# Performance work log

Measured on AMD Instinct MI355X. Metric: run time of the kernel, lower is better.

Reference implementation:

```python
import jax, jax.numpy as jnp
import numpy as np

ALPHA = 0.2  # leaky relu slope
NEG_BIG = -9000000000000000.0


def setup_inputs() -> dict:
    key = jax.random.key(0)
    k1, k2, k3, k4 = jax.random.split(key, 4)
    B, N, Fin, Fout = 8, 2048, 256, 256
    h = jax.random.normal(k1, (B, N, Fin), dtype=jnp.float32)
    adj = jax.random.randint(k2, (B, N, N), 0, 2, dtype=jnp.int32)
    # xavier_uniform with gain=1.414
    gain = 1.414
    limW = gain * np.sqrt(6.0 / (Fin + Fout))
    W = jax.random.uniform(k3, (Fin, Fout), dtype=jnp.float32, minval=-limW, maxval=limW)
    lima = gain * np.sqrt(6.0 / (2 * Fout + 1))
    a = jax.random.uniform(k4, (2 * Fout, 1), dtype=jnp.float32, minval=-lima, maxval=lima)
    return {"h": h, "adj": adj, "W": W, "a": a}


def reference(h, adj, W, a):
    # Wh: [B, N, F]
    Wh = jnp.matmul(h, W)
    Fout = W.shape[1]
    a1 = a[:Fout, 0]   # scores for source node i (repeat_interleave side)
    a2 = a[Fout:, 0]   # scores for target node j (repeat side)
    # e[b,i,j] = leakyrelu(Wh[b,i]@a1 + Wh[b,j]@a2)  -- decomposed, no O(N^2 * 2F) tensor
    s1 = jnp.einsum('bnf,f->bn', Wh, a1)  # [B, N]
    s2 = jnp.einsum('bnf,f->bn', Wh, a2)  # [B, N]
    e = jax.nn.leaky_relu(s1[:, :, None] + s2[:, None, :], negative_slope=ALPHA)
    masked = jnp.where(adj > 0, e, jnp.full_like(e, NEG_BIG))
    attention = jax.nn.softmax(masked, axis=2)  # dropout=0 (eval mode)
    h_prime = jnp.matmul(attention, Wh)  # [B, N, F]
    return jax.nn.elu(h_prime)
```

## Files before the change

kernel.cpp:

```cpp
#include <hip/hip_runtime.h>

typedef __attribute__((ext_vector_type(8))) short bhalf8;
typedef __attribute__((ext_vector_type(4))) float floatx4;

#define ALPHA_LR 0.2f

__device__ __forceinline__ unsigned short f2bf(float f) {
  union { float f; unsigned int u; } v; v.f = f;
  unsigned int r = v.u + 0x7fffu + ((v.u >> 16) & 1u);
  return (unsigned short)(r >> 16);
}
__device__ __forceinline__ float bf2f(unsigned short u) {
  union { unsigned int u; float f; } v; v.u = ((unsigned int)u) << 16;
  return v.f;
}
__device__ __forceinline__ void gld16(const void* g, void* l) {
  __builtin_amdgcn_global_load_lds((const __attribute__((address_space(1))) unsigned int*)g,
                                   (__attribute__((address_space(3))) unsigned int*)l,
                                   16, 0, 0);
}

__global__ void k0w_split(const float* __restrict__ W,
                          unsigned short* __restrict__ WThi,
                          unsigned short* __restrict__ WTlo,
                          unsigned int* __restrict__ s2maxEnc) {
  __shared__ float s[16][17];
  const int tx = threadIdx.x, ty = threadIdx.y;
  if (blockIdx.x == 0 && blockIdx.y == 0 && ty == 0 && tx < 8) s2maxEnc[tx] = 0u;
  const int n0 = blockIdx.x * 16, k0 = blockIdx.y * 16;
  s[ty][tx] = W[(k0 + ty) * 256 + n0 + tx];
  __syncthreads();
  float v = s[tx][ty];
  const int k = k0 + tx, n = n0 + ty;
  unsigned short hi = f2bf(v);
  unsigned short lo = f2bf(v - bf2f(hi));
  const int idx = (k >> 5) * 8192 + n * 32 + (k & 31);
  WThi[idx] = hi;
  WTlo[idx] = lo;
}

__global__ __launch_bounds__(512, 2) void k1_mfma(const float* __restrict__ h,
                                                  const unsigned short* __restrict__ Bhi_g,
                                                  const unsigned short* __restrict__ Blo_g,
                                                  const float* __restrict__ a_g,
                                                  unsigned short* __restrict__ WhPack,
                                                  float* __restrict__ s1,
                                                  float* __restrict__ s2,
                                                  unsigned int* __restrict__ s2maxEnc) {
  __shared__ unsigned short Ah[64 * 264], Al[64 * 264];
  __shared__ unsigned short Bh[2][8192], Bl[2][8192];
  __shared__ float s1red[64], s2red[64];
  const int t = threadIdx.x;
  const long r0 = (long)blockIdx.x * 64;
  const int wave = t >> 6, lane = t & 63;

  if (t < 64) { s1red[t] = 0.f; s2red[t] = 0.f; }

#pragma unroll
  for (int rep = 0; rep < 2; rep++) {
    const int off = wave * 1024 + rep * 512;
    gld16(Bhi_g + off + lane * 8, &Bh[0][off]);
    gld16(Blo_g + off + lane * 8, &Bl[0][off]);
  }

#pragma unroll
  for (int q = 0; q < 8; q++) {
    int idx = q * 512 + t;
    int row = idx >> 6, c4 = idx & 63;
    float4 x = *(const float4*)(h + (r0 + row) * 256 + c4 * 4);
    float xs[4] = {x.x, x.y, x.z, x.w};
    unsigned short hs[4], ls[4];
#pragma unroll
    for (int qq = 0; qq < 4; qq++) {
      hs[qq] = f2bf(xs[qq]);
      ls[qq] = f2bf(xs[qq] - bf2f(hs[qq]));
    }
    *(ushort4*)&Ah[row * 264 + c4 * 4] = (ushort4){hs[0], hs[1], hs[2], hs[3]};
    *(ushort4*)&Al[row * 264 + c4 * 4] = (ushort4){ls[0], ls[1], ls[2], ls[3]};
  }
  __syncthreads();

  const int wm = wave >> 2, wn = wave & 3;
  const int lhi = lane >> 4, llo = lane & 15;

  floatx4 acc[2][4];
#pragma unroll
  for (int mt = 0; mt < 2; mt++)
#pragma unroll
    for (int nt = 0; nt < 4; nt++) acc[mt][nt] = (floatx4){0.f, 0.f, 0.f, 0.f};

  for (int ks = 0; ks < 8; ks++) {
    const int cur = ks & 1, nxt = cur ^ 1, ksn = (ks + 1) & 7;
#pragma unroll
    for (int rep = 0; rep < 2; rep++) {
      const int off = wave * 1024 + rep * 512;
      gld16(Bhi_g + ksn * 8192 + off + lane * 8, &Bh[nxt][off]);
      gld16(Blo_g + ksn * 8192 + off + lane * 8, &Bl[nxt][off]);
    }

    const int k0 = ks * 32;
    bhalf8 ah[2], al[2], bh[4], bl[4];
#pragma unroll
    for (int mt = 0; mt < 2; mt++) {
      int ro = (wm * 32 + mt * 16 + llo) * 264 + k0 + lhi * 8;
      ah[mt] = *(const bhalf8*)&Ah[ro];
      al[mt] = *(const bhalf8*)&Al[ro];
    }
#pragma unroll
    for (int nt = 0; nt < 4; nt++) {
      int ro = (wn * 64 + nt * 16 + llo) * 32 + lhi * 8;
      bh[nt] = *(const bhalf8*)&Bh[cur][ro];
      bl[nt] = *(const bhalf8*)&Bl[cur][ro];
    }
#pragma unroll
    for (int mt = 0; mt < 2; mt++)
#pragma unroll
      for (int nt = 0; nt < 4; nt++) {
        acc[mt][nt] = __builtin_amdgcn_mfma_f32_16x16x32_bf16(ah[mt], bh[nt], acc[mt][nt], 0, 0, 0);
        acc[mt][nt] = __builtin_amdgcn_mfma_f32_16x16x32_bf16(ah[mt], bl[nt], acc[mt][nt], 0, 0, 0);
        acc[mt][nt] = __builtin_amdgcn_mfma_f32_16x16x32_bf16(al[mt], bh[nt], acc[mt][nt], 0, 0, 0);
      }
    __syncthreads();
  }

  float a1v[4], a2v[4];
#pragma unroll
  for (int nt = 0; nt < 4; nt++) {
    int f = wn * 64 + nt * 16 + llo;
    a1v[nt] = a_g[f];
    a2v[nt] = a_g[256 + f];
  }

  const int b = (int)(r0 >> 11);
  const int jt_base = (int)((r0 & 2047) >> 5);

#pragma unroll
  for (int mt = 0; mt < 2; mt++) {
    float p1[4], p2[4];
#pragma unroll
    for (int reg = 0; reg < 4; reg++) {
      p1[reg] = acc[mt][0][reg] * a1v[0] + acc[mt][1][reg] * a1v[1] +
                acc[mt][2][reg] * a1v[2] + acc[mt][3][reg] * a1v[3];
      p2[reg] = acc[mt][0][reg] * a2v[0] + acc[mt][1][reg] * a2v[1] +
                acc[mt][2][reg] * a2v[2] + acc[mt][3][reg] * a2v[3];
    }
#pragma unroll
    for (int off = 1; off < 16; off <<= 1) {
#pragma unroll
      for (int reg = 0; reg < 4; reg++) {
        p1[reg] += __shfl_xor(p1[reg], off);
        p2[reg] += __shfl_xor(p2[reg], off);
      }
    }
    if (llo == 0) {
#pragma unroll
      for (int reg = 0; reg < 4; reg++) {
        int il = wm * 32 + mt * 16 + lhi * 4 + reg;
        atomicAdd(&s1red[il], p1[reg]);
        atomicAdd(&s2red[il], p2[reg]);
      }
    }
#pragma unroll
    for (int nt = 0; nt < 4; nt++) {
      int f = wn * 64 + nt * 16 + llo;
      int jt = jt_base + wm;
      ushort4 pk = (ushort4){f2bf(acc[mt][nt][0]), f2bf(acc[mt][nt][1]),
                             f2bf(acc[mt][nt][2]), f2bf(acc[mt][nt][3])};
      *(ushort4*)&WhPack[((long)((b * 64 + jt) * 256 + f)) * 32 + mt * 16 + lhi * 4] = pk;
    }
  }

  __syncthreads();
  if (t < 64) {
    s1[r0 + t] = s1red[t];
    s2[r0 + t] = s2red[t];
    float v = s2red[t];
#pragma unroll
    for (int o = 32; o; o >>= 1) v = fmaxf(v, __shfl_xor(v, o));
    if (t == 0) {
      unsigned int u = __float_as_uint(v);
      unsigned int key = (u & 0x80000000u) ? ~u : (u | 0x80000000u);
      atomicMax(s2maxEnc + b, key);
    }
  }
}

__global__ __launch_bounds__(512, 4) void k3_attn(const unsigned short* __restrict__ WhPack,
                                                  const int* __restrict__ adj,
                                                  const float* __restrict__ s1g,
                                                  const float* __restrict__ s2g,
                                                  const unsigned int* __restrict__ s2maxEnc,
                                                  float* __restrict__ out) {
  const int t = threadIdx.x;
  const int i0 = blockIdx.x * 32;
  const int b = blockIdx.y;
  const long gr0 = (long)b * 2048 + i0;

  __shared__ float s2all[2048];
  __shared__ unsigned short WhT[2][8192];
  __shared__ unsigned short P[2][1280];
  __shared__ float lvv[32];

  ((float4*)s2all)[t] = ((const float4*)(s2g + (long)b * 2048))[t];

  const int wave = t >> 6, lane = t & 63;
  const int wm = wave >> 2, wn = wave & 3;
  const int lhi = lane >> 4, llo = lane & 15;
  const int i_p = t >> 4;
  const int jl0 = (t & 15) * 2;

  const float s1i = s1g[gr0 + i_p];
  const unsigned int ek = s2maxEnc[b];
  const float s2max = (ek & 0x80000000u) ? __uint_as_float(ek & 0x7fffffffu)
                                         : __uint_as_float(~ek);
  const float xm = s1i + s2max;
  const float Mi = fmaxf(xm, ALPHA_LR * xm);

  const int* aptr = adj + (gr0 + i_p) * 2048 + jl0;
  const unsigned short* tbase = WhPack + ((long)b * 64) * 8192;

#pragma unroll
  for (int rep = 0; rep < 2; rep++) {
    const int off = wave * 1024 + rep * 512;
    gld16(tbase + off + lane * 8, &WhT[0][off]);
  }
  int2 aj0 = *(const int2*)aptr;
  int2 aj1 = *(const int2*)(aptr + 32);

  __syncthreads();

  float lsum;
  {
    float x0 = s1i + s2all[jl0];
    float x1 = s1i + s2all[jl0 + 1];
    x0 = fmaxf(x0, ALPHA_LR * x0);
    x1 = fmaxf(x1, ALPHA_LR * x1);
    float e0 = (aj0.x > 0) ? __expf(x0 - Mi) : 0.f;
    float e1 = (aj0.y > 0) ? __expf(x1 - Mi) : 0.f;
    lsum = e0 + e1;
    *(unsigned int*)&P[0][i_p * 40 + jl0] =
        (unsigned)f2bf(e0) | ((unsigned)f2bf(e1) << 16);
  }
  __syncthreads();

  floatx4 acc[4];
#pragma unroll
  for (int nt = 0; nt < 4; nt++) acc[nt] = (floatx4){0.f, 0.f, 0.f, 0.f};

  for (int jt = 0; jt < 64; jt++) {
    const int cur = jt & 1, nxt = cur ^ 1;
    if (jt < 63) {
      const int jtn = jt + 1;
#pragma unroll
      for (int rep = 0; rep < 2; rep++) {
        const int off = wave * 1024 + rep * 512;
        gld16(tbase + jtn * 8192 + off + lane * 8, &WhT[nxt][off]);
      }
      const int2 ajc = aj1;
      const int jpf = (jt + 2 < 64) ? jt + 2 : 63;
      aj1 = *(const int2*)(aptr + jpf * 32);
      float x0 = s1i + s2all[jtn * 32 + jl0];
      float x1 = s1i + s2all[jtn * 32 + jl0 + 1];
      x0 = fmaxf(x0, ALPHA_LR * x0);
      x1 = fmaxf(x1, ALPHA_LR * x1);
      float e0 = (ajc.x > 0) ? __expf(x0 - Mi) : 0.f;
      float e1 = (ajc.y > 0) ? __expf(x1 - Mi) : 0.f;
      lsum += e0 + e1;
      *(unsigned int*)&P[nxt][i_p * 40 + jl0] =
          (unsigned)f2bf(e0) | ((unsigned)f2bf(e1) << 16);
    }
    bhalf8 af = *(const bhalf8*)&P[cur][(wm * 16 + llo) * 40 + lhi * 8];
    bhalf8 bf[4];
#pragma unroll
    for (int nt = 0; nt < 4; nt++)
      bf[nt] = *(const bhalf8*)&WhT[cur][(wn * 64 + nt * 16 + llo) * 32 + lhi * 8];
#pragma unroll
    for (int nt = 0; nt < 4; nt++)
      acc[nt] = __builtin_amdgcn_mfma_f32_16x16x32_bf16(af, bf[nt], acc[nt], 0, 0, 0);
    __syncthreads();
  }

  lsum += __shfl_xor(lsum, 1);
  lsum += __shfl_xor(lsum, 2);
  lsum += __shfl_xor(lsum, 4);
  lsum += __shfl_xor(lsum, 8);
  if ((t & 15) == 0) lvv[i_p] = 1.f / fmaxf(lsum, 1e-35f);
  __syncthreads();

#pragma unroll
  for (int nt = 0; nt < 4; nt++) {
#pragma unroll
    for (int reg = 0; reg < 4; reg++) {
      int il = wm * 16 + lhi * 4 + reg;
      int f = wn * 64 + nt * 16 + llo;
      float v = acc[nt][reg] * lvv[il];
      v = v > 0.f ? v : expm1f(v);
      out[(gr0 + il) * 256 + f] = v;
    }
  }
}

extern "C" void kernel_launch(void* const* d_in, const int* in_sizes, int n_in,
                              void* d_out, int out_size, void* d_ws, size_t ws_size,
                              hipStream_t stream) {
  const float* h = (const float*)d_in[0];
  const int* adj = (const int*)d_in[1];
  const float* W = (const float*)d_in[2];
  const float* a = (const float*)d_in[3];
  float* out = (float*)d_out;

  char* ws = (char*)d_ws;
  unsigned short* WhPack = (unsigned short*)ws;
  unsigned short* WThi = (unsigned short*)(ws + 8388608);
  unsigned short* WTlo = (unsigned short*)(ws + 8519680);
  float* s1 = (float*)(ws + 8650752);
  float* s2 = (float*)(ws + 8716288);
  unsigned int* s2maxEnc = (unsigned int*)(ws + 8781824);

  hipLaunchKernelGGL(k0w_split, dim3(16, 16), dim3(16, 16), 0, stream, W, WThi, WTlo, s2maxEnc);
  hipLaunchKernelGGL(k1_mfma, dim3(256), dim3(512), 0, stream, h, WThi, WTlo, a,
                     WhPack, s1, s2, s2maxEnc);
  hipLaunchKernelGGL(k3_attn, dim3(64, 8), dim3(512), 0, stream, WhPack, adj,
                     s1, s2, s2maxEnc, out);
}
```

Before: 253.4 us.

## Restructure attention kernel to compute P in registers and stream Wh directly

The attention kernel drops the shared-memory staging of Wh tiles and the P probability tile. Each wave now owns 16 rows and 128 output features. It builds its bf16 A-operand for the MFMA directly in registers from adj and the scores, and double-buffers the B fragments loaded from global memory into registers. The per-step __syncthreads barriers go away and blocks cover 64 rows, halving the grid. The cost is more global/L2 traffic for Wh, since each wave loads its own fragments and adj/scores are computed redundantly across the two feature halves. bf16 conversion changes from rounding to truncation, which slightly alters precision.

```diff
diff --git a/kernel.cpp b/kernel.cpp
--- a/kernel.cpp
+++ b/kernel.cpp
@@ -185,117 +185,105 @@
   }
 }
 
-__global__ __launch_bounds__(512, 4) void k3_attn(const unsigned short* __restrict__ WhPack,
+__global__ __launch_bounds__(512, 2) void k3_attn(const unsigned short* __restrict__ WhPack,
                                                   const int* __restrict__ adj,
                                                   const float* __restrict__ s1g,
                                                   const float* __restrict__ s2g,
                                                   const unsigned int* __restrict__ s2maxEnc,
                                                   float* __restrict__ out) {
   const int t = threadIdx.x;
-  const int i0 = blockIdx.x * 32;
   const int b = blockIdx.y;
-  const long gr0 = (long)b * 2048 + i0;
+  const int wave = t >> 6, lane = t & 63;
+  const int llo = lane & 15, lhi = lane >> 4;
+  const int fc = wave >> 2;
+  const int rg = wave & 3;
+  const long gr0 = (long)b * 2048 + blockIdx.x * 64 + rg * 16;
 
   __shared__ float s2all[2048];
-  __shared__ unsigned short WhT[2][8192];
-  __shared__ unsigned short P[2][1280];
-  __shared__ float lvv[32];
-
   ((float4*)s2all)[t] = ((const float4*)(s2g + (long)b * 2048))[t];
 
-  const int wave = t >> 6, lane = t & 63;
-  const int wm = wave >> 2, wn = wave & 3;
-  const int lhi = lane >> 4, llo = lane & 15;
-  const int i_p = t >> 4;
-  const int jl0 = (t & 15) * 2;
-
-  const float s1i = s1g[gr0 + i_p];
+  const float s1i = s1g[gr0 + llo];
   const unsigned int ek = s2maxEnc[b];
   const float s2max = (ek & 0x80000000u) ? __uint_as_float(ek & 0x7fffffffu)
                                          : __uint_as_float(~ek);
   const float xm = s1i + s2max;
   const float Mi = fmaxf(xm, ALPHA_LR * xm);
 
-  const int* aptr = adj + (gr0 + i_p) * 2048 + jl0;
-  const unsigned short* tbase = WhPack + ((long)b * 64) * 8192;
-
-#pragma unroll
-  for (int rep = 0; rep < 2; rep++) {
-    const int off = wave * 1024 + rep * 512;
-    gld16(tbase + off + lane * 8, &WhT[0][off]);
-  }
-  int2 aj0 = *(const int2*)aptr;
-  int2 aj1 = *(const int2*)(aptr + 32);
+  const int* aptr = adj + (gr0 + llo) * 2048 + lhi * 8;
+  const unsigned short* Bp =
+      WhPack + (long)b * 64 * 8192 + (fc * 128 + llo) * 32 + lhi * 8;
 
   __syncthreads();
 
-  float lsum;
-  {
-    float x0 = s1i + s2all[jl0];
-    float x1 = s1i + s2all[jl0 + 1];
-    x0 = fmaxf(x0, ALPHA_LR * x0);
-    x1 = fmaxf(x1, ALPHA_LR * x1);
-    float e0 = (aj0.x > 0) ? __expf(x0 - Mi) : 0.f;
-    float e1 = (aj0.y > 0) ? __expf(x1 - Mi) : 0.f;
-    lsum = e0 + e1;
-    *(unsigned int*)&P[0][i_p * 40 + jl0] =
-        (unsigned)f2bf(e0) | ((unsigned)f2bf(e1) << 16);
-  }
-  __syncthreads();
-
-  floatx4 acc[4];
-#pragma unroll
-  for (int nt = 0; nt < 4; nt++) acc[nt] = (floatx4){0.f, 0.f, 0.f, 0.f};
-
-  for (int jt = 0; jt < 64; jt++) {
-    const int cur = jt & 1, nxt = cur ^ 1;
-    if (jt < 63) {
-      const int jtn = jt + 1;
-#pragma unroll
-      for (int rep = 0; rep < 2; rep++) {
-        const int off = wave * 1024 + rep * 512;
-        gld16(tbase + jtn * 8192 + off + lane * 8, &WhT[nxt][off]);
-      }
-      const int2 ajc = aj1;
-      const int jpf = (jt + 2 < 64) ? jt + 2 : 63;
-      aj1 = *(const int2*)(aptr + jpf * 32);
-      float x0 = s1i + s2all[jtn * 32 + jl0];
-      float x1 = s1i + s2all[jtn * 32 + jl0 + 1];
-      x0 = fmaxf(x0, ALPHA_LR * x0);
-      x1 = fmaxf(x1, ALPHA_LR * x1);
-      float e0 = (ajc.x > 0) ? __expf(x0 - Mi) : 0.f;
-      float e1 = (ajc.y > 0) ? __expf(x1 - Mi) : 0.f;
-      lsum += e0 + e1;
-      *(unsigned int*)&P[nxt][i_p * 40 + jl0] =
-          (unsigned)f2bf(e0) | ((unsigned)f2bf(e1) << 16);
-    }
-    bhalf8 af = *(const bhalf8*)&P[cur][(wm * 16 + llo) * 40 + lhi * 8];
-    bhalf8 bf[4];
-#pragma unroll
-    for (int nt = 0; nt < 4; nt++)
-      bf[nt] = *(const bhalf8*)&WhT[cur][(wn * 64 + nt * 16 + llo) * 32 + lhi * 8];
-#pragma unroll
-    for (int nt = 0; nt < 4; nt++)
-      acc[nt] = __builtin_amdgcn_mfma_f32_16x16x32_bf16(af, bf[nt], acc[nt], 0, 0, 0);
-    __syncthreads();
-  }
-
-  lsum += __shfl_xor(lsum, 1);
-  lsum += __shfl_xor(lsum, 2);
-  lsum += __shfl_xor(lsum, 4);
-  lsum += __shfl_xor(lsum, 8);
-  if ((t & 15) == 0) lvv[i_p] = 1.f / fmaxf(lsum, 1e-35f);
-  __syncthreads();
-
-#pragma unroll
-  for (int nt = 0; nt < 4; nt++) {
-#pragma unroll
-    for (int reg = 0; reg < 4; reg++) {
-      int il = wm * 16 + lhi * 4 + reg;
-      int f = wn * 64 + nt * 16 + llo;
-      float v = acc[nt][reg] * lvv[il];
+  floatx4 acc[8];
+#pragma unroll
+  for (int nt = 0; nt < 8; nt++) acc[nt] = (floatx4){0.f, 0.f, 0.f, 0.f};
+
+  bhalf8 B0[8], B1[8];
+  int4 ajq[2][2];
+  ajq[0][0] = *(const int4*)(aptr);
+  ajq[0][1] = *(const int4*)(aptr + 4);
+  ajq[1][0] = *(const int4*)(aptr + 32);
+  ajq[1][1] = *(const int4*)(aptr + 36);
+#pragma unroll
+  for (int nt = 0; nt < 8; nt++) B0[nt] = *(const bhalf8*)(Bp + nt * 512);
+
+  float lsum = 0.f;
+
+#define K3_STEP(JT, BCUR, BNXT)                                                \
+  {                                                                            \
+    const int jt_ = (JT);                                                      \
+    const int cb = jt_ & 1;                                                    \
+                                                      \
+    const unsigned short* bn = Bp + ((jt_ + 1 < 64) ? jt_ + 1 : 63) * 8192;    \
+    _Pragma("unroll") for (int nt = 0; nt < 8; nt++)                           \
+        BNXT[nt] = *(const bhalf8*)(bn + nt * 512);                            \
+                                   \
+    int4 a0_ = ajq[cb][0], a1_ = ajq[cb][1];                                   \
+    const int jp_ = (jt_ + 2 < 64) ? jt_ + 2 : 63;                             \
+    ajq[cb][0] = *(const int4*)(aptr + jp_ * 32);                              \
+    ajq[cb][1] = *(const int4*)(aptr + jp_ * 32 + 4);                          \
+    int am_[8] = {a0_.x, a0_.y, a0_.z, a0_.w, a1_.x, a1_.y, a1_.z, a1_.w};     \
+    float4 sa_ = *(const float4*)&s2all[jt_ * 32 + lhi * 8];                   \
+    float4 sb_ = *(const float4*)&s2all[jt_ * 32 + lhi * 8 + 4];               \
+    float sv_[8] = {sa_.x, sa_.y, sa_.z, sa_.w, sb_.x, sb_.y, sb_.z, sb_.w};   \
+    union { unsigned int u[4]; bhalf8 v; } au_;                                \
+    _Pragma("unroll") for (int p = 0; p < 4; p++) {                            \
+      float x0 = s1i + sv_[2 * p];                                             \
+      float x1 = s1i + sv_[2 * p + 1];                                         \
+      x0 = fmaxf(x0, ALPHA_LR * x0);                                           \
+      x1 = fmaxf(x1, ALPHA_LR * x1);                                           \
+      float e0 = (am_[2 * p] > 0) ? __expf(x0 - Mi) : 0.f;                     \
+      float e1 = (am_[2 * p + 1] > 0) ? __expf(x1 - Mi) : 0.f;                 \
+      lsum += e0 + e1;                                                         \
+      union { float f; unsigned int u; } u0_, u1_;                             \
+      u0_.f = e0; u1_.f = e1;                                                  \
+      au_.u[p] = (u0_.u >> 16) | (u1_.u & 0xffff0000u);                        \
+    }                                                                          \
+    _Pragma("unroll") for (int nt = 0; nt < 8; nt++)                           \
+        acc[nt] = __builtin_amdgcn_mfma_f32_16x16x32_bf16(au_.v, BCUR[nt],     \
+                                                          acc[nt], 0, 0, 0);   \
+  }
+
+  for (int jt = 0; jt < 64; jt += 2) {
+    K3_STEP(jt, B0, B1)
+    K3_STEP(jt + 1, B1, B0)
+  }
+#undef K3_STEP
+
+  lsum += __shfl_xor(lsum, 16);
+  lsum += __shfl_xor(lsum, 32);
+  const float linv = 1.f / fmaxf(lsum, 1e-35f);
+
+#pragma unroll
+  for (int reg = 0; reg < 4; reg++) {
+    const float lr = __shfl(linv, lhi * 4 + reg);
+    const int row = lhi * 4 + reg;
+#pragma unroll
+    for (int nt = 0; nt < 8; nt++) {
+      float v = acc[nt][reg] * lr;
       v = v > 0.f ? v : expm1f(v);
-      out[(gr0 + il) * 256 + f] = v;
+      out[(gr0 + row) * 256 + fc * 128 + nt * 16 + llo] = v;
     }
   }
 }
@@ -320,6 +308,6 @@
   hipLaunchKernelGGL(k0w_split, dim3(16, 16), dim3(16, 16), 0, stream, W, WThi, WTlo, s2maxEnc);
   hipLaunchKernelGGL(k1_mfma, dim3(256), dim3(512), 0, stream, h, WThi, WTlo, a,
                      WhPack, s1, s2, s2maxEnc);
-  hipLaunchKernelGGL(k3_attn, dim3(64, 8), dim3(512), 0, stream, WhPack, adj,
+  hipLaunchKernelGGL(k3_attn, dim3(32, 8), dim3(512), 0, stream, WhPack, adj,
                      s1, s2, s2maxEnc, out);
 }
```

Result: slower. 344.8 us (+36.1%).

## Deepen Wh tile prefetch to four stages with XOR-swizzled LDS and adj ring

Applied to the files above, without the earlier changes.

Grows the Wh tile LDS ring from double to quad buffering, issuing global-to-LDS loads three tiles ahead, and keeps a four-deep register ring of adjacency loads. The LDS layout of Wh tiles is XOR-swizzled on the load side and matched on the read side to reduce bank conflicts. The per-iteration __syncthreads is replaced by a partial vmcnt wait plus a raw barrier so later loads can stay in flight. This doubles the LDS footprint, which may cut occupancy, and the waitcnt encoding must match the number of outstanding loads to stay correct.

```diff
diff --git a/kernel.cpp b/kernel.cpp
--- a/kernel.cpp
+++ b/kernel.cpp
@@ -197,7 +197,7 @@
   const long gr0 = (long)b * 2048 + i0;
 
   __shared__ float s2all[2048];
-  __shared__ unsigned short WhT[2][8192];
+  __shared__ unsigned short WhT[4][8192];
   __shared__ unsigned short P[2][1280];
   __shared__ float lvv[32];
 
@@ -218,18 +218,23 @@
 
   const int* aptr = adj + (gr0 + i_p) * 2048 + jl0;
   const unsigned short* tbase = WhPack + ((long)b * 64) * 8192;
-
-#pragma unroll
-  for (int rep = 0; rep < 2; rep++) {
-    const int off = wave * 1024 + rep * 512;
-    gld16(tbase + off + lane * 8, &WhT[0][off]);
-  }
-  int2 aj0 = *(const int2*)aptr;
-  int2 aj1 = *(const int2*)(aptr + 32);
-
-  __syncthreads();
-
-  float lsum;
+  const int laneoff = (lane >> 2) * 32 + (((lane & 3) ^ ((lane >> 3) & 3)) * 8);
+  const int segoff = wave * 1024;
+
+#pragma unroll
+  for (int tile = 0; tile < 3; tile++)
+#pragma unroll
+    for (int rep = 0; rep < 2; rep++) {
+      const int off = segoff + rep * 512;
+      gld16(tbase + tile * 8192 + off + laneoff, &WhT[tile][off]);
+    }
+  const int2 aj0 = *(const int2*)aptr;
+  int2 ajbuf[4];
+#pragma unroll
+  for (int q = 1; q <= 4; q++) ajbuf[q & 3] = *(const int2*)(aptr + q * 32);
+  __syncthreads();
+
+  float lsum = 0.f;
   {
     float x0 = s1i + s2all[jl0];
     float x1 = s1i + s2all[jl0 + 1];
@@ -238,8 +243,7 @@
     float e0 = (aj0.x > 0) ? __expf(x0 - Mi) : 0.f;
     float e1 = (aj0.y > 0) ? __expf(x1 - Mi) : 0.f;
     lsum = e0 + e1;
-    *(unsigned int*)&P[0][i_p * 40 + jl0] =
-        (unsigned)f2bf(e0) | ((unsigned)f2bf(e1) << 16);
+    *(unsigned int*)&P[0][i_p * 40 + jl0] = (unsigned)f2bf(e0) | ((unsigned)f2bf(e1) << 16);
   }
   __syncthreads();
 
@@ -247,18 +251,24 @@
 #pragma unroll
   for (int nt = 0; nt < 4; nt++) acc[nt] = (floatx4){0.f, 0.f, 0.f, 0.f};
 
+  const int baseB = (wn * 64 + llo) * 32 + ((lhi ^ ((llo >> 1) & 3)) * 8);
+  const int aoff = (wm * 16 + llo) * 40 + lhi * 8;
+
   for (int jt = 0; jt < 64; jt++) {
-    const int cur = jt & 1, nxt = cur ^ 1;
+    const int cur = jt & 3;
+    if (jt < 61) {
+      const int ld = (jt + 3) & 3;
+      const long gb = (long)(jt + 3) * 8192;
+#pragma unroll
+      for (int rep = 0; rep < 2; rep++) {
+        const int off = segoff + rep * 512;
+        gld16(tbase + gb + off + laneoff, &WhT[ld][off]);
+      }
+    }
     if (jt < 63) {
       const int jtn = jt + 1;
-#pragma unroll
-      for (int rep = 0; rep < 2; rep++) {
-        const int off = wave * 1024 + rep * 512;
-        gld16(tbase + jtn * 8192 + off + lane * 8, &WhT[nxt][off]);
-      }
-      const int2 ajc = aj1;
-      const int jpf = (jt + 2 < 64) ? jt + 2 : 63;
-      aj1 = *(const int2*)(aptr + jpf * 32);
+      const int2 ajc = ajbuf[jtn & 3];
+      if (jt < 59) ajbuf[(jt + 5) & 3] = *(const int2*)(aptr + (jt + 5) * 32);
       float x0 = s1i + s2all[jtn * 32 + jl0];
       float x1 = s1i + s2all[jtn * 32 + jl0 + 1];
       x0 = fmaxf(x0, ALPHA_LR * x0);
@@ -266,18 +276,19 @@
       float e0 = (ajc.x > 0) ? __expf(x0 - Mi) : 0.f;
       float e1 = (ajc.y > 0) ? __expf(x1 - Mi) : 0.f;
       lsum += e0 + e1;
-      *(unsigned int*)&P[nxt][i_p * 40 + jl0] =
+      *(unsigned int*)&P[jtn & 1][i_p * 40 + jl0] =
           (unsigned)f2bf(e0) | ((unsigned)f2bf(e1) << 16);
     }
-    bhalf8 af = *(const bhalf8*)&P[cur][(wm * 16 + llo) * 40 + lhi * 8];
+    bhalf8 af = *(const bhalf8*)&P[jt & 1][aoff];
     bhalf8 bf[4];
 #pragma unroll
     for (int nt = 0; nt < 4; nt++)
-      bf[nt] = *(const bhalf8*)&WhT[cur][(wn * 64 + nt * 16 + llo) * 32 + lhi * 8];
+      bf[nt] = *(const bhalf8*)&WhT[cur][baseB + nt * 512];
 #pragma unroll
     for (int nt = 0; nt < 4; nt++)
       acc[nt] = __builtin_amdgcn_mfma_f32_16x16x32_bf16(af, bf[nt], acc[nt], 0, 0, 0);
-    __syncthreads();
+    __builtin_amdgcn_s_waitcnt(0x76);
+    __builtin_amdgcn_s_barrier();
   }
 
   lsum += __shfl_xor(lsum, 1);
```

Result: slower. 311.8 us (+23.0%).
